# Kernel optimization log

Measured on AMD Instinct MI355X. Metric: run time of the kernel, lower is better.

The kernel has to match this reference:

```python
import jax, jax.numpy as jnp
import numpy as np

B, H, W, C = 4, 64, 64, 1280
NH = 16          # num heads
HD = C // NH     # 80 features per head
WS = 14          # window size
REL = 2 * WS - 1 # 27 relative-position entries per axis
EPS = 1e-6


def setup_inputs() -> dict:
    key = jax.random.key(0)
    ks = jax.random.split(key, 16)
    s = 0.02
    return {
        "imagelike_bhwc": jax.random.normal(ks[0], (B, H, W, C), jnp.float32),
        "ln1_g": jnp.ones((C,), jnp.float32),
        "ln1_b": jnp.zeros((C,), jnp.float32),
        "qkv_w": jax.random.normal(ks[1], (C, 3 * C), jnp.float32) * s,
        "qkv_b": jnp.zeros((3 * C,), jnp.float32),
        "proj_w": jax.random.normal(ks[2], (C, C), jnp.float32) * s,
        "proj_b": jnp.zeros((C,), jnp.float32),
        "rel_pos_h": jax.random.normal(ks[3], (REL, HD), jnp.float32) * s,
        "rel_pos_w": jax.random.normal(ks[4], (REL, HD), jnp.float32) * s,
        "ln2_g": jnp.ones((C,), jnp.float32),
        "ln2_b": jnp.zeros((C,), jnp.float32),
        "mlp_w1": jax.random.normal(ks[5], (C, 4 * C), jnp.float32) * s,
        "mlp_b1": jnp.zeros((4 * C,), jnp.float32),
        "mlp_w2": jax.random.normal(ks[6], (4 * C, C), jnp.float32) * s,
        "mlp_b2": jnp.zeros((C,), jnp.float32),
    }


def _layernorm(t, g, b):
    mu = jnp.mean(t, axis=-1, keepdims=True)
    var = jnp.var(t, axis=-1, keepdims=True)
    return (t - mu) * jax.lax.rsqrt(var + EPS) * g + b


def reference(imagelike_bhwc, ln1_g, ln1_b, qkv_w, qkv_b, proj_w, proj_b,
              rel_pos_h, rel_pos_w, ln2_g, ln2_b, mlp_w1, mlp_b1, mlp_w2, mlp_b2):
    x = imagelike_bhwc
    b, h, w, c = x.shape
    hd = c // NH
    scale = hd ** -0.5
    # --- image -> windows (pad to multiple of WS) ---
    hp, wp = (-h) % WS, (-w) % WS
    xp = jnp.pad(x, ((0, 0), (0, hp), (0, wp), (0, 0)))
    Hp, Wp = h + hp, w + wp
    ny, nx = Hp // WS, Wp // WS
    win = xp.reshape(b, ny, WS, nx, WS, c).transpose(0, 1, 3, 2, 4, 5)
    win = win.reshape(b * ny * nx, WS, WS, c)      # (Bw, S, S, C)
    Bw, N = win.shape[0], WS * WS
    # --- pre-attention layernorm + qkv ---
    t = _layernorm(win, ln1_g, ln1_b)
    qkv = t.reshape(Bw, N, c) @ qkv_w + qkv_b      # (Bw, N, 3C)
    qkv = qkv.reshape(Bw, N, 3, NH, hd).transpose(2, 0, 3, 1, 4)  # (3,Bw,NH,N,hd)
    q, k, v = qkv[0], qkv[1], qkv[2]
    # --- scores + decomposed relative position bias ---
    attn = jnp.einsum('bhqd,bhkd->bhqk', q * scale, k)            # (Bw,NH,N,N)
    idx = jnp.arange(WS)[:, None] - jnp.arange(WS)[None, :] + (WS - 1)
    Rh = rel_pos_h[idx]                                           # (WS,WS,hd)
    Rw = rel_pos_w[idx]                                           # (WS,WS,hd)
    qr = q.reshape(Bw, NH, WS, WS, hd)
    bias_h = jnp.einsum('bnyxd,ykd->bnyxk', qr, Rh)               # (Bw,NH,WS,WS,WS)
    bias_w = jnp.einsum('bnyxd,xkd->bnyxk', qr, Rw)
    bias = (bias_h[..., :, None] + bias_w[..., None, :]).reshape(Bw, NH, N, N)
    attn = jax.nn.softmax(attn + bias, axis=-1)
    out = jnp.einsum('bhqk,bhkd->bhqd', attn, v)                  # (Bw,NH,N,hd)
    out = out.transpose(0, 2, 1, 3).reshape(Bw, WS, WS, c)
    out = out @ proj_w + proj_b
    attn_out = out + win                                          # residual 1
    # --- MLP ---
    t2 = _layernorm(attn_out, ln2_g, ln2_b)
    mlp = jax.nn.gelu(t2 @ mlp_w1 + mlp_b1, approximate=False) @ mlp_w2 + mlp_b2
    out = mlp + attn_out                                          # residual 2
    # --- windows -> image (remove padding) ---
    img = out.reshape(b, ny, nx, WS, WS, c).transpose(0, 1, 3, 2, 4, 5)
    img = img.reshape(b, Hp, Wp, c)
    return img[:, :h, :w, :]
```

## Files before the change

### kernel.cpp

```cpp
#include <hip/hip_runtime.h>

typedef __attribute__((ext_vector_type(8))) short short8;
typedef __attribute__((ext_vector_type(4))) float f32x4;

#define GLBP(p) ((const __attribute__((address_space(1))) void*)(p))
#define LDSP(p) ((__attribute__((address_space(3))) void*)(p))

__device__ __forceinline__ float bf2f(unsigned short u) {
  return __uint_as_float(((unsigned int)u) << 16);
}
__device__ __forceinline__ unsigned short f2bf(float f) {
  unsigned int u = __float_as_uint(f);
  u += 0x7fff + ((u >> 16) & 1);
  return (unsigned short)(u >> 16);
}

__device__ __forceinline__ void tok2pix(int gt, int& b, int& py, int& px) {
  int w = gt / 196, t = gt - w * 196;
  b = w / 25;
  int wr = w - b * 25;
  int wy = wr / 5, wx = wr - wy * 5;
  int ty = t / 14;
  py = wy * 14 + ty;
  px = wx * 14 + (t - ty * 14);
}

__global__ void k_transpose(const float* __restrict__ W, unsigned short* __restrict__ Wt,
                            int K, int N) {
  __shared__ float tile[32][33];
  int tx = threadIdx.x, ty = threadIdx.y;
  int n0 = blockIdx.x * 32, k0 = blockIdx.y * 32;
#pragma unroll
  for (int i = 0; i < 4; ++i)
    tile[ty + 8 * i][tx] = W[(size_t)(k0 + ty + 8 * i) * N + n0 + tx];
  __syncthreads();
#pragma unroll
  for (int i = 0; i < 4; ++i)
    Wt[(size_t)(n0 + ty + 8 * i) * K + k0 + tx] = f2bf(tile[tx][ty + 8 * i]);
}

__global__ __launch_bounds__(256) void k_ln1(const float* __restrict__ x,
                                             const float* __restrict__ g,
                                             const float* __restrict__ be,
                                             unsigned short* __restrict__ A1,
                                             int w0, int ctok) {
  int m = blockIdx.x * 4 + (threadIdx.x >> 6);
  int lane = threadIdx.x & 63;
  int b, py, px;
  tok2pix(w0 * 196 + m, b, py, px);
  bool valid = (m < ctok) && (py < 64) && (px < 64);
  const float* row = x + ((size_t)((b * 64 + py) * 64 + px)) * 1280;
  float v[20];
#pragma unroll
  for (int i = 0; i < 20; ++i) v[i] = valid ? row[lane + 64 * i] : 0.f;
  float s = 0.f, ss = 0.f;
#pragma unroll
  for (int i = 0; i < 20; ++i) { s += v[i]; ss += v[i] * v[i]; }
#pragma unroll
  for (int o = 32; o > 0; o >>= 1) { s += __shfl_down(s, o); ss += __shfl_down(ss, o); }
  s = __shfl(s, 0);
  ss = __shfl(ss, 0);
  float mu = s * (1.f / 1280.f);
  float var = ss * (1.f / 1280.f) - mu * mu;
  float rinv = rsqrtf(var + 1e-6f);
  unsigned short* o1 = A1 + (size_t)m * 1280;
#pragma unroll
  for (int i = 0; i < 20; ++i) {
    int c = lane + 64 * i;
    o1[c] = f2bf((v[i] - mu) * rinv * g[c] + be[c]);
  }
}

__global__ __launch_bounds__(256) void k_ln2(const float* __restrict__ AT,
                                             const float* __restrict__ g,
                                             const float* __restrict__ be,
                                             unsigned short* __restrict__ A2,
                                             int w0, int ctok) {
  int m = blockIdx.x * 4 + (threadIdx.x >> 6);
  int lane = threadIdx.x & 63;
  int b, py, px;
  tok2pix(w0 * 196 + m, b, py, px);
  bool valid = (m < ctok) && (py < 64) && (px < 64);
  const float* row = AT + ((size_t)((b * 64 + py) * 64 + px)) * 1280;
  float v[20];
#pragma unroll
  for (int i = 0; i < 20; ++i) v[i] = valid ? row[lane + 64 * i] : 0.f;
  float s = 0.f, ss = 0.f;
#pragma unroll
  for (int i = 0; i < 20; ++i) { s += v[i]; ss += v[i] * v[i]; }
#pragma unroll
  for (int o = 32; o > 0; o >>= 1) { s += __shfl_down(s, o); ss += __shfl_down(ss, o); }
  s = __shfl(s, 0);
  ss = __shfl(ss, 0);
  float mu = s * (1.f / 1280.f);
  float var = ss * (1.f / 1280.f) - mu * mu;
  float rinv = rsqrtf(var + 1e-6f);
  unsigned short* o1 = A2 + (size_t)m * 1280;
#pragma unroll
  for (int i = 0; i < 20; ++i) {
    int c = lane + 64 * i;
    o1[c] = f2bf((v[i] - mu) * rinv * g[c] + be[c]);
  }
}

template <int EPI>
__device__ __forceinline__ void gemm_body(const unsigned short* __restrict__ A,
                                          const unsigned short* __restrict__ Bt,
                                          int K, int N, int gx,
                                          const float* __restrict__ bias,
                                          void* __restrict__ outp, int ctok) {
  __shared__ __align__(16) char smem[73728];
  int tid = threadIdx.x;
  int w = tid >> 6, lane = tid & 63;
  int nwg = gridDim.x, bid = blockIdx.x;
  int q = nwg >> 3, r = nwg & 7;
  int xcd = bid & 7, loc = bid >> 3;
  int wg = (xcd < r ? xcd * (q + 1) : r * (q + 1) + (xcd - r) * q) + loc;
  int bx = wg % gx, by = wg / gx;
  int mBase = by * 256, nBase = bx * 128;
  int wr = w >> 2, wc = w & 3;
  int la = lane & 15, lg = lane >> 4;

  int srow = tid >> 2;
  int schunk = (tid & 3) ^ ((srow >> 1) & 3);
  const char* pa0 = (const char*)A + (size_t)(mBase + srow) * K * 2 + (schunk << 4);
  const char* pa1 = (const char*)A + (size_t)(mBase + 128 + srow) * K * 2 + (schunk << 4);
  const char* pb0 = (const char*)Bt + (size_t)(nBase + srow) * K * 2 + (schunk << 4);
  int ldst = tid * 16;

  auto STAGE = [&](int slot, size_t ko) {
    int b = slot * 24576;
    __builtin_amdgcn_global_load_lds(GLBP(pa0 + ko), LDSP(smem + b + ldst), 16, 0, 0);
    __builtin_amdgcn_global_load_lds(GLBP(pa1 + ko), LDSP(smem + b + 8192 + ldst), 16, 0, 0);
    __builtin_amdgcn_global_load_lds(GLBP(pb0 + ko), LDSP(smem + b + 16384 + ldst), 16, 0, 0);
  };

  int offA[8], offB[2];
#pragma unroll
  for (int m = 0; m < 8; ++m) {
    int rr = wr * 128 + m * 16 + la;
    offA[m] = rr * 64 + ((lg ^ ((rr >> 1) & 3)) << 4);
  }
#pragma unroll
  for (int n = 0; n < 2; ++n) {
    int rr = wc * 32 + n * 16 + la;
    offB[n] = 16384 + rr * 64 + ((lg ^ ((rr >> 1) & 3)) << 4);
  }

  const f32x4 z4 = {0.f, 0.f, 0.f, 0.f};
  f32x4 acc[8][2];
#pragma unroll
  for (int m = 0; m < 8; ++m)
#pragma unroll
    for (int n = 0; n < 2; ++n) acc[m][n] = z4;

  int NT = K >> 5;
  STAGE(0, 0);
  STAGE(1, 64);
  int rs = 0;
  for (int t = 0; t < NT; ++t) {
    if (t + 1 < NT)
      asm volatile("s_waitcnt vmcnt(3)" ::: "memory");
    else
      asm volatile("s_waitcnt vmcnt(0)" ::: "memory");
    __builtin_amdgcn_s_barrier();
    __builtin_amdgcn_sched_barrier(0);
    if (t + 2 < NT) {
      int ws = rs + 2;
      if (ws >= 3) ws -= 3;
      STAGE(ws, (size_t)(t + 2) * 64);
    }
    const char* buf = (const char*)smem + rs * 24576;
    short8 af[4], bfr[2];
#pragma unroll
    for (int n = 0; n < 2; ++n) bfr[n] = *(const short8*)(buf + offB[n]);
#pragma unroll
    for (int m = 0; m < 4; ++m) af[m] = *(const short8*)(buf + offA[m]);
    __builtin_amdgcn_s_setprio(1);
#pragma unroll
    for (int m = 0; m < 4; ++m)
#pragma unroll
      for (int n = 0; n < 2; ++n)
        acc[m][n] = __builtin_amdgcn_mfma_f32_16x16x32_bf16(af[m], bfr[n], acc[m][n], 0, 0, 0);
    __builtin_amdgcn_s_setprio(0);
    __builtin_amdgcn_sched_barrier(0);
#pragma unroll
    for (int m = 0; m < 4; ++m) af[m] = *(const short8*)(buf + offA[m + 4]);
    __builtin_amdgcn_s_setprio(1);
#pragma unroll
    for (int m = 0; m < 4; ++m)
#pragma unroll
      for (int n = 0; n < 2; ++n)
        acc[m + 4][n] = __builtin_amdgcn_mfma_f32_16x16x32_bf16(af[m], bfr[n], acc[m + 4][n], 0, 0, 0);
    __builtin_amdgcn_s_setprio(0);
    rs = (rs == 2) ? 0 : rs + 1;
  }

#pragma unroll
  for (int m = 0; m < 8; ++m) {
#pragma unroll
    for (int n = 0; n < 2; ++n) {
      int col = nBase + wc * 32 + n * 16 + la;
      float bcol = bias[col];
#pragma unroll
      for (int j = 0; j < 4; ++j) {
        int row = mBase + wr * 128 + m * 16 + lg * 4 + j;
        float v = acc[m][n][j] + bcol;
        if (EPI == 0) {
          if (row < ctok) {
            int wloc = row / 196, tt = row - wloc * 196;
            int which = col / 1280, cr = col - which * 1280;
            int nh = cr / 80, d = cr - nh * 80;
            ((unsigned short*)outp)[((((size_t)wloc * 16 + nh) * 3 + which) * 196 + tt) * 80 + d] =
                f2bf(v);
          }
        } else {
          float gg = 0.5f * v * (1.f + erff(v * 0.70710678118654752f));
          ((unsigned short*)outp)[(size_t)row * N + col] = f2bf(gg);
        }
      }
    }
  }
}

template <int EPI>
__device__ __forceinline__ void gemm128_body(const unsigned short* __restrict__ A,
                                             const unsigned short* __restrict__ Bt,
                                             int K, int N, int gx,
                                             const float* __restrict__ bias,
                                             float* __restrict__ outp,
                                             const float* __restrict__ xres,
                                             int w0, int ctok) {
  __shared__ __align__(16) char smem[49152];
  int tid = threadIdx.x;
  int w = tid >> 6, lane = tid & 63;
  int nwg = gridDim.x, bid = blockIdx.x;
  int q = nwg >> 3, r = nwg & 7;
  int xcd = bid & 7, loc = bid >> 3;
  int wg = (xcd < r ? xcd * (q + 1) : r * (q + 1) + (xcd - r) * q) + loc;
  int bx = wg % gx, by = wg / gx;
  int mBase = by * 128, nBase = bx * 128;
  int wr = w >> 1, wc = w & 1;
  int la = lane & 15, lg = lane >> 4;

  int srow = tid >> 2;
  int schunk = (tid & 3) ^ ((srow >> 1) & 3);
  const char* pa[2];
  const char* pb[2];
#pragma unroll
  for (int i = 0; i < 2; ++i) {
    pa[i] = (const char*)A + (size_t)(mBase + srow + i * 64) * K * 2 + (schunk << 4);
    pb[i] = (const char*)Bt + (size_t)(nBase + srow + i * 64) * K * 2 + (schunk << 4);
  }
  int ldst = tid * 16;

  auto STAGE = [&](int slot, size_t ko) {
    int b = slot * 16384;
#pragma unroll
    for (int i = 0; i < 2; ++i)
      __builtin_amdgcn_global_load_lds(GLBP(pa[i] + ko), LDSP(smem + b + i * 4096 + ldst), 16, 0, 0);
#pragma unroll
    for (int i = 0; i < 2; ++i)
      __builtin_amdgcn_global_load_lds(GLBP(pb[i] + ko), LDSP(smem + b + 8192 + i * 4096 + ldst), 16, 0, 0);
  };

  int offA[4], offB[4];
#pragma unroll
  for (int m = 0; m < 4; ++m) {
    int rr = wr * 64 + m * 16 + la;
    offA[m] = rr * 64 + ((lg ^ ((rr >> 1) & 3)) << 4);
  }
#pragma unroll
  for (int n = 0; n < 4; ++n) {
    int rr = wc * 64 + n * 16 + la;
    offB[n] = 8192 + rr * 64 + ((lg ^ ((rr >> 1) & 3)) << 4);
  }

  const f32x4 z4 = {0.f, 0.f, 0.f, 0.f};
  f32x4 acc[4][4];
#pragma unroll
  for (int m = 0; m < 4; ++m)
#pragma unroll
    for (int n = 0; n < 4; ++n) acc[m][n] = z4;

  int NT = K >> 5;
  STAGE(0, 0);
  STAGE(1, 64);
  int rs = 0;
  for (int t = 0; t < NT; ++t) {
    if (t + 1 < NT)
      asm volatile("s_waitcnt vmcnt(4)" ::: "memory");
    else
      asm volatile("s_waitcnt vmcnt(0)" ::: "memory");
    __builtin_amdgcn_s_barrier();
    __builtin_amdgcn_sched_barrier(0);
    if (t + 2 < NT) {
      int ws = rs + 2;
      if (ws >= 3) ws -= 3;
      STAGE(ws, (size_t)(t + 2) * 64);
    }
    const char* buf = (const char*)smem + rs * 16384;
    short8 af[4], bfr[4];
#pragma unroll
    for (int n = 0; n < 4; ++n) bfr[n] = *(const short8*)(buf + offB[n]);
#pragma unroll
    for (int m = 0; m < 4; ++m) af[m] = *(const short8*)(buf + offA[m]);
    __builtin_amdgcn_s_setprio(1);
#pragma unroll
    for (int m = 0; m < 4; ++m)
#pragma unroll
      for (int n = 0; n < 4; ++n)
        acc[m][n] = __builtin_amdgcn_mfma_f32_16x16x32_bf16(af[m], bfr[n], acc[m][n], 0, 0, 0);
    __builtin_amdgcn_s_setprio(0);
    rs = (rs == 2) ? 0 : rs + 1;
  }

#pragma unroll
  for (int m = 0; m < 4; ++m) {
#pragma unroll
    for (int n = 0; n < 4; ++n) {
      int col = nBase + wc * 64 + n * 16 + la;
      float bcol = bias[col];
#pragma unroll
      for (int j = 0; j < 4; ++j) {
        int row = mBase + wr * 64 + m * 16 + lg * 4 + j;
        if (row < ctok) {
          int b, py, px;
          tok2pix(w0 * 196 + row, b, py, px);
          if (py < 64 && px < 64) {
            size_t pix = ((size_t)((b * 64 + py) * 64 + px)) * 1280 + col;
            float v = acc[m][n][j] + bcol;
            if (EPI == 1)
              outp[pix] = v + xres[pix];
            else
              outp[pix] = v + outp[pix];
          }
        }
      }
    }
  }
}

__global__ __launch_bounds__(512, 4) void k_gqkv(const unsigned short* A, const unsigned short* Bt,
                                                 int K, int N, int gx, const float* bias, void* o,
                                                 int ct) {
  gemm_body<0>(A, Bt, K, N, gx, bias, o, ct);
}
__global__ __launch_bounds__(512, 4) void k_gmlp1(const unsigned short* A, const unsigned short* Bt,
                                                  int K, int N, int gx, const float* bias, void* o,
                                                  int ct) {
  gemm_body<2>(A, Bt, K, N, gx, bias, o, ct);
}
__global__ __launch_bounds__(256, 3) void k_gproj(const unsigned short* A, const unsigned short* Bt,
                                                  int K, int N, int gx, const float* bias, float* o,
                                                  const float* xr, int w0, int ct) {
  gemm128_body<1>(A, Bt, K, N, gx, bias, o, xr, w0, ct);
}
__global__ __launch_bounds__(256, 3) void k_gmlp2(const unsigned short* A, const unsigned short* Bt,
                                                  int K, int N, int gx, const float* bias, float* o,
                                                  const float* xr, int w0, int ct) {
  gemm128_body<3>(A, Bt, K, N, gx, bias, o, xr, w0, ct);
}

__global__ __launch_bounds__(512, 1) void k_attn(const unsigned short* __restrict__ qkv,
                                                 const float* __restrict__ rph,
                                                 const float* __restrict__ rpw,
                                                 unsigned short* __restrict__ AO) {
  __shared__ unsigned short Ks[208 * 104];
  __shared__ unsigned short Vt[80 * 232];
  __shared__ unsigned short Ps[8][16 * 232];
  __shared__ unsigned short Bls[196 * 28];
  int wh = blockIdx.x;
  int w = wh >> 4, nh = wh & 15;
  int tid = threadIdx.x, wid = tid >> 6, lane = tid & 63;
  int la = lane & 15, lg = lane >> 4;
  const unsigned short* qb = qkv + (size_t)wh * 47040;
  const unsigned short* kb = qb + 15680;
  const unsigned short* vb = qb + 31360;
  const short8 z8 = {0, 0, 0, 0, 0, 0, 0, 0};

  for (int c = tid; c < 208 * 13; c += 512) {
    int t = c / 13, seg = c - t * 13;
    short8 kv = z8;
    if (t < 196 && seg < 10) kv = *(const short8*)(kb + (size_t)t * 80 + seg * 8);
    *(short8*)(Ks + t * 104 + seg * 8) = kv;
  }
  for (int c = tid; c < 1960; c += 512) {
    int t = c / 10, d8 = (c - t * 10) * 8;
    short8 vv = *(const short8*)(vb + (size_t)t * 80 + d8);
#pragma unroll
    for (int e = 0; e < 8; ++e) Vt[(d8 + e) * 232 + t] = (unsigned short)vv[e];
  }
  for (int i = tid; i < 80 * 36; i += 512) Vt[(i / 36) * 232 + 196 + (i % 36)] = 0;
  for (int id = tid; id < 196 * 28; id += 512) {
    int t = id / 28, c = id - t * 28;
    int y = t / 14, xx = t - y * 14;
    const float* R = (c < 14) ? (rph + (size_t)(y - c + 13) * 80)
                              : (rpw + (size_t)(xx - (c - 14) + 13) * 80);
    const unsigned short* qq = qb + (size_t)t * 80;
    float acc = 0.f;
#pragma unroll
    for (int d8 = 0; d8 < 10; ++d8) {
      short8 qv = *(const short8*)(qq + d8 * 8);
      const float4* Rv = (const float4*)(R + d8 * 8);
      float4 ra = Rv[0], rb = Rv[1];
      acc += bf2f((unsigned short)qv[0]) * ra.x + bf2f((unsigned short)qv[1]) * ra.y +
             bf2f((unsigned short)qv[2]) * ra.z + bf2f((unsigned short)qv[3]) * ra.w +
             bf2f((unsigned short)qv[4]) * rb.x + bf2f((unsigned short)qv[5]) * rb.y +
             bf2f((unsigned short)qv[6]) * rb.z + bf2f((unsigned short)qv[7]) * rb.w;
    }
    Bls[id] = f2bf(acc);
  }
  __syncthreads();

  int kyv[13], kxv[13];
#pragma unroll
  for (int ci = 0; ci < 13; ++ci) {
    int key = ci * 16 + la;
    kyv[ci] = key / 14;
    kxv[ci] = key - kyv[ci] * 14;
  }

  const float scale = 0.111803398874989485f;
  const f32x4 z4 = {0.f, 0.f, 0.f, 0.f};
  unsigned short* P = Ps[wid];

  auto process = [&](int rb) {
    short8 qa[3];
    int tq = rb * 16 + la;
    if (tq >= 196) tq = 0;
#pragma unroll
    for (int kk = 0; kk < 3; ++kk) {
      int d = kk * 32 + lg * 8;
      qa[kk] = (kk < 2 || lg < 2) ? *(const short8*)(qb + (size_t)tq * 80 + d) : z8;
    }
    f32x4 s[13];
#pragma unroll
    for (int i = 0; i < 13; ++i) s[i] = z4;
#pragma unroll
    for (int kk = 0; kk < 3; ++kk) {
#pragma unroll
      for (int ni = 0; ni < 13; ++ni) {
        short8 bb = *(const short8*)(Ks + (ni * 16 + la) * 104 + kk * 32 + lg * 8);
        s[ni] = __builtin_amdgcn_mfma_f32_16x16x32_bf16(qa[kk], bb, s[ni], 0, 0, 0);
      }
    }
#pragma unroll
    for (int j = 0; j < 4; ++j) {
      int rloc = lg * 4 + j;
      int t = rb * 16 + rloc;
      bool tval = t < 196;
      const unsigned short* Bp = Bls + (tval ? t : 0) * 28;
      float v[13];
      float mx = -3e30f;
#pragma unroll
      for (int ci = 0; ci < 13; ++ci) {
        int key = ci * 16 + la;
        float val = s[ci][j] * scale;
        if (key < 196 && tval) val += bf2f(Bp[kyv[ci]]) + bf2f(Bp[14 + kxv[ci]]);
        if (key >= 196 || !tval) val = -3e30f;
        v[ci] = val;
        mx = fmaxf(mx, val);
      }
#pragma unroll
      for (int o = 1; o < 16; o <<= 1) mx = fmaxf(mx, __shfl_xor(mx, o));
      float sum = 0.f;
#pragma unroll
      for (int ci = 0; ci < 13; ++ci) {
        float e = __expf(v[ci] - mx);
        v[ci] = e;
        sum += e;
      }
#pragma unroll
      for (int o = 1; o < 16; o <<= 1) sum += __shfl_xor(sum, o);
      float inv = 1.f / sum;
#pragma unroll
      for (int ci = 0; ci < 13; ++ci) P[rloc * 232 + ci * 16 + la] = f2bf(v[ci] * inv);
      P[rloc * 232 + 208 + la] = 0;
    }
    f32x4 o5[5];
#pragma unroll
    for (int i = 0; i < 5; ++i) o5[i] = z4;
#pragma unroll
    for (int kc = 0; kc < 7; ++kc) {
      short8 aa = *(const short8*)(P + la * 232 + kc * 32 + lg * 8);
#pragma unroll
      for (int ni = 0; ni < 5; ++ni) {
        short8 bb = *(const short8*)(Vt + (ni * 16 + la) * 232 + kc * 32 + lg * 8);
        o5[ni] = __builtin_amdgcn_mfma_f32_16x16x32_bf16(aa, bb, o5[ni], 0, 0, 0);
      }
    }
#pragma unroll
    for (int ni = 0; ni < 5; ++ni)
#pragma unroll
      for (int j = 0; j < 4; ++j) {
        int t = rb * 16 + lg * 4 + j;
        if (t < 196)
          AO[((size_t)w * 196 + t) * 1280 + nh * 80 + ni * 16 + la] = f2bf(o5[ni][j]);
      }
  };

  process(wid);
  if (wid < 5) process(wid + 8);
}

extern "C" void kernel_launch(void* const* d_in, const int* in_sizes, int n_in,
                              void* d_out, int out_size, void* d_ws, size_t ws_size,
                              hipStream_t stream) {
  const float* x = (const float*)d_in[0];
  const float* ln1g = (const float*)d_in[1];
  const float* ln1b = (const float*)d_in[2];
  const float* qkvw = (const float*)d_in[3];
  const float* qkvb = (const float*)d_in[4];
  const float* projw = (const float*)d_in[5];
  const float* projb = (const float*)d_in[6];
  const float* rph = (const float*)d_in[7];
  const float* rpw = (const float*)d_in[8];
  const float* ln2g = (const float*)d_in[9];
  const float* ln2b = (const float*)d_in[10];
  const float* w1 = (const float*)d_in[11];
  const float* b1 = (const float*)d_in[12];
  const float* w2 = (const float*)d_in[13];
  const float* b2 = (const float*)d_in[14];
  float* out = (float*)d_out;

  const size_t woff = (3840ull * 1280 + 1280ull * 1280 + 5120ull * 1280 + 1280ull * 5120) * 2;
  const int NWopts[12] = {25, 20, 18, 16, 14, 12, 10, 8, 5, 4, 2, 1};
  int NW = 0, Mb = 0;
  for (int i = 0; i < 12; ++i) {
    int nw = NWopts[i];
    int mb = ((nw * 196 + 255) / 256) * 256;
    size_t tot = woff + (size_t)mb * 12800;
    if (tot <= ws_size) { NW = nw; Mb = mb; break; }
  }
  if (!NW) return;

  char* p = (char*)d_ws;
  unsigned short* qkvwT = (unsigned short*)p; p += 3840ull * 1280 * 2;
  unsigned short* projwT = (unsigned short*)p; p += 1280ull * 1280 * 2;
  unsigned short* w1T = (unsigned short*)p; p += 5120ull * 1280 * 2;
  unsigned short* w2T = (unsigned short*)p; p += 1280ull * 5120 * 2;
  unsigned short* A1 = (unsigned short*)p; p += (size_t)Mb * 2560;
  unsigned short* QKV = (unsigned short*)p; p += (size_t)Mb * 7680;
  unsigned short* AO = (unsigned short*)p;
  unsigned short* Hb = QKV;
  unsigned short* A2 = A1;

  k_transpose<<<dim3(120, 40), dim3(32, 8), 0, stream>>>(qkvw, qkvwT, 1280, 3840);
  k_transpose<<<dim3(40, 40), dim3(32, 8), 0, stream>>>(projw, projwT, 1280, 1280);
  k_transpose<<<dim3(160, 40), dim3(32, 8), 0, stream>>>(w1, w1T, 1280, 5120);
  k_transpose<<<dim3(40, 160), dim3(32, 8), 0, stream>>>(w2, w2T, 5120, 1280);

  int gy256 = Mb / 256, gy128 = Mb / 128;
  int nchunks = (100 + NW - 1) / NW;
  for (int c = 0; c < nchunks; ++c) {
    int w0 = c * NW;
    int cw = (100 - w0 < NW) ? (100 - w0) : NW;
    int ctok = cw * 196;
    k_ln1<<<Mb / 4, 256, 0, stream>>>(x, ln1g, ln1b, A1, w0, ctok);
    k_gqkv<<<30 * gy256, 512, 0, stream>>>(A1, qkvwT, 1280, 3840, 30, qkvb, (void*)QKV, ctok);
    k_attn<<<cw * 16, 512, 0, stream>>>(QKV, rph, rpw, AO);
    k_gproj<<<10 * gy128, 256, 0, stream>>>(AO, projwT, 1280, 1280, 10, projb, out, x, w0, ctok);
    k_ln2<<<Mb / 4, 256, 0, stream>>>(out, ln2g, ln2b, A2, w0, ctok);
    k_gmlp1<<<40 * gy256, 512, 0, stream>>>(A2, w1T, 1280, 5120, 40, b1, (void*)Hb, ctok);
    k_gmlp2<<<10 * gy128, 256, 0, stream>>>(Hb, w2T, 5120, 1280, 10, b2, out, nullptr, w0, ctok);
  }
}
```

Measured before the change: 1.873 ms.

## Unify GEMMs on 128x128 tiles and split-K proj/mlp2 with atomic residual accumulation

Drops the 256x128 GEMM body and routes the qkv and mlp1 GEMMs through the 128x128 kernel. The proj GEMM now uses split-K 2 and mlp2 uses split-K 4, adding partial sums into the output with float atomicAdd. LN1 pre-writes x into the output buffer as the residual base, so the proj epilogue no longer reads x. This raises the workgroup count for the narrow N=1280 GEMMs to improve occupancy, at the cost of atomic traffic, nondeterministic summation order and smaller tiles on the wide GEMMs.

```diff
diff --git a/kernel.cpp b/kernel.cpp
--- a/kernel.cpp
+++ b/kernel.cpp
@@ -43,13 +43,15 @@
                                              const float* __restrict__ g,
                                              const float* __restrict__ be,
                                              unsigned short* __restrict__ A1,
+                                             float* __restrict__ outinit,
                                              int w0, int ctok) {
   int m = blockIdx.x * 4 + (threadIdx.x >> 6);
   int lane = threadIdx.x & 63;
   int b, py, px;
   tok2pix(w0 * 196 + m, b, py, px);
   bool valid = (m < ctok) && (py < 64) && (px < 64);
-  const float* row = x + ((size_t)((b * 64 + py) * 64 + px)) * 1280;
+  size_t pixrow = ((size_t)((b * 64 + py) * 64 + px)) * 1280;
+  const float* row = x + pixrow;
   float v[20];
 #pragma unroll
   for (int i = 0; i < 20; ++i) v[i] = valid ? row[lane + 64 * i] : 0.f;
@@ -64,10 +66,12 @@
   float var = ss * (1.f / 1280.f) - mu * mu;
   float rinv = rsqrtf(var + 1e-6f);
   unsigned short* o1 = A1 + (size_t)m * 1280;
+  float* oi = outinit + pixrow;
 #pragma unroll
   for (int i = 0; i < 20; ++i) {
     int c = lane + 64 * i;
     o1[c] = f2bf((v[i] - mu) * rinv * g[c] + be[c]);
+    if (valid) oi[c] = v[i];
   }
 }
 
@@ -103,133 +107,12 @@
   }
 }
 
-template <int EPI>
-__device__ __forceinline__ void gemm_body(const unsigned short* __restrict__ A,
-                                          const unsigned short* __restrict__ Bt,
-                                          int K, int N, int gx,
-                                          const float* __restrict__ bias,
-                                          void* __restrict__ outp, int ctok) {
-  __shared__ __align__(16) char smem[73728];
-  int tid = threadIdx.x;
-  int w = tid >> 6, lane = tid & 63;
-  int nwg = gridDim.x, bid = blockIdx.x;
-  int q = nwg >> 3, r = nwg & 7;
-  int xcd = bid & 7, loc = bid >> 3;
-  int wg = (xcd < r ? xcd * (q + 1) : r * (q + 1) + (xcd - r) * q) + loc;
-  int bx = wg % gx, by = wg / gx;
-  int mBase = by * 256, nBase = bx * 128;
-  int wr = w >> 2, wc = w & 3;
-  int la = lane & 15, lg = lane >> 4;
-
-  int srow = tid >> 2;
-  int schunk = (tid & 3) ^ ((srow >> 1) & 3);
-  const char* pa0 = (const char*)A + (size_t)(mBase + srow) * K * 2 + (schunk << 4);
-  const char* pa1 = (const char*)A + (size_t)(mBase + 128 + srow) * K * 2 + (schunk << 4);
-  const char* pb0 = (const char*)Bt + (size_t)(nBase + srow) * K * 2 + (schunk << 4);
-  int ldst = tid * 16;
-
-  auto STAGE = [&](int slot, size_t ko) {
-    int b = slot * 24576;
-    __builtin_amdgcn_global_load_lds(GLBP(pa0 + ko), LDSP(smem + b + ldst), 16, 0, 0);
-    __builtin_amdgcn_global_load_lds(GLBP(pa1 + ko), LDSP(smem + b + 8192 + ldst), 16, 0, 0);
-    __builtin_amdgcn_global_load_lds(GLBP(pb0 + ko), LDSP(smem + b + 16384 + ldst), 16, 0, 0);
-  };
-
-  int offA[8], offB[2];
-#pragma unroll
-  for (int m = 0; m < 8; ++m) {
-    int rr = wr * 128 + m * 16 + la;
-    offA[m] = rr * 64 + ((lg ^ ((rr >> 1) & 3)) << 4);
-  }
-#pragma unroll
-  for (int n = 0; n < 2; ++n) {
-    int rr = wc * 32 + n * 16 + la;
-    offB[n] = 16384 + rr * 64 + ((lg ^ ((rr >> 1) & 3)) << 4);
-  }
-
-  const f32x4 z4 = {0.f, 0.f, 0.f, 0.f};
-  f32x4 acc[8][2];
-#pragma unroll
-  for (int m = 0; m < 8; ++m)
-#pragma unroll
-    for (int n = 0; n < 2; ++n) acc[m][n] = z4;
-
-  int NT = K >> 5;
-  STAGE(0, 0);
-  STAGE(1, 64);
-  int rs = 0;
-  for (int t = 0; t < NT; ++t) {
-    if (t + 1 < NT)
-      asm volatile("s_waitcnt vmcnt(3)" ::: "memory");
-    else
-      asm volatile("s_waitcnt vmcnt(0)" ::: "memory");
-    __builtin_amdgcn_s_barrier();
-    __builtin_amdgcn_sched_barrier(0);
-    if (t + 2 < NT) {
-      int ws = rs + 2;
-      if (ws >= 3) ws -= 3;
-      STAGE(ws, (size_t)(t + 2) * 64);
-    }
-    const char* buf = (const char*)smem + rs * 24576;
-    short8 af[4], bfr[2];
-#pragma unroll
-    for (int n = 0; n < 2; ++n) bfr[n] = *(const short8*)(buf + offB[n]);
-#pragma unroll
-    for (int m = 0; m < 4; ++m) af[m] = *(const short8*)(buf + offA[m]);
-    __builtin_amdgcn_s_setprio(1);
-#pragma unroll
-    for (int m = 0; m < 4; ++m)
-#pragma unroll
-      for (int n = 0; n < 2; ++n)
-        acc[m][n] = __builtin_amdgcn_mfma_f32_16x16x32_bf16(af[m], bfr[n], acc[m][n], 0, 0, 0);
-    __builtin_amdgcn_s_setprio(0);
-    __builtin_amdgcn_sched_barrier(0);
-#pragma unroll
-    for (int m = 0; m < 4; ++m) af[m] = *(const short8*)(buf + offA[m + 4]);
-    __builtin_amdgcn_s_setprio(1);
-#pragma unroll
-    for (int m = 0; m < 4; ++m)
-#pragma unroll
-      for (int n = 0; n < 2; ++n)
-        acc[m + 4][n] = __builtin_amdgcn_mfma_f32_16x16x32_bf16(af[m], bfr[n], acc[m + 4][n], 0, 0, 0);
-    __builtin_amdgcn_s_setprio(0);
-    rs = (rs == 2) ? 0 : rs + 1;
-  }
-
-#pragma unroll
-  for (int m = 0; m < 8; ++m) {
-#pragma unroll
-    for (int n = 0; n < 2; ++n) {
-      int col = nBase + wc * 32 + n * 16 + la;
-      float bcol = bias[col];
-#pragma unroll
-      for (int j = 0; j < 4; ++j) {
-        int row = mBase + wr * 128 + m * 16 + lg * 4 + j;
-        float v = acc[m][n][j] + bcol;
-        if (EPI == 0) {
-          if (row < ctok) {
-            int wloc = row / 196, tt = row - wloc * 196;
-            int which = col / 1280, cr = col - which * 1280;
-            int nh = cr / 80, d = cr - nh * 80;
-            ((unsigned short*)outp)[((((size_t)wloc * 16 + nh) * 3 + which) * 196 + tt) * 80 + d] =
-                f2bf(v);
-          }
-        } else {
-          float gg = 0.5f * v * (1.f + erff(v * 0.70710678118654752f));
-          ((unsigned short*)outp)[(size_t)row * N + col] = f2bf(gg);
-        }
-      }
-    }
-  }
-}
-
-template <int EPI>
+template <int EPI, int SPLITK>
 __device__ __forceinline__ void gemm128_body(const unsigned short* __restrict__ A,
                                              const unsigned short* __restrict__ Bt,
-                                             int K, int N, int gx,
+                                             int Ktot, int N, int gx,
                                              const float* __restrict__ bias,
-                                             float* __restrict__ outp,
-                                             const float* __restrict__ xres,
+                                             void* __restrict__ outp,
                                              int w0, int ctok) {
   __shared__ __align__(16) char smem[49152];
   int tid = threadIdx.x;
@@ -238,8 +121,12 @@
   int q = nwg >> 3, r = nwg & 7;
   int xcd = bid & 7, loc = bid >> 3;
   int wg = (xcd < r ? xcd * (q + 1) : r * (q + 1) + (xcd - r) * q) + loc;
-  int bx = wg % gx, by = wg / gx;
+  int ntiles = nwg / SPLITK;
+  int kslice = wg / ntiles, tile = wg - kslice * ntiles;
+  int bx = tile % gx, by = tile / gx;
   int mBase = by * 128, nBase = bx * 128;
+  int K = Ktot / SPLITK;
+  int k0elem = kslice * K;
   int wr = w >> 1, wc = w & 1;
   int la = lane & 15, lg = lane >> 4;
 
@@ -249,8 +136,8 @@
   const char* pb[2];
 #pragma unroll
   for (int i = 0; i < 2; ++i) {
-    pa[i] = (const char*)A + (size_t)(mBase + srow + i * 64) * K * 2 + (schunk << 4);
-    pb[i] = (const char*)Bt + (size_t)(nBase + srow + i * 64) * K * 2 + (schunk << 4);
+    pa[i] = (const char*)A + ((size_t)(mBase + srow + i * 64) * Ktot + k0elem) * 2 + (schunk << 4);
+    pb[i] = (const char*)Bt + ((size_t)(nBase + srow + i * 64) * Ktot + k0elem) * 2 + (schunk << 4);
   }
   int ldst = tid * 16;
 
@@ -320,20 +207,28 @@
 #pragma unroll
     for (int n = 0; n < 4; ++n) {
       int col = nBase + wc * 64 + n * 16 + la;
-      float bcol = bias[col];
+      float bcol = (SPLITK == 1 || kslice == 0) ? bias[col] : 0.f;
 #pragma unroll
       for (int j = 0; j < 4; ++j) {
         int row = mBase + wr * 64 + m * 16 + lg * 4 + j;
-        if (row < ctok) {
-          int b, py, px;
-          tok2pix(w0 * 196 + row, b, py, px);
-          if (py < 64 && px < 64) {
-            size_t pix = ((size_t)((b * 64 + py) * 64 + px)) * 1280 + col;
-            float v = acc[m][n][j] + bcol;
-            if (EPI == 1)
-              outp[pix] = v + xres[pix];
-            else
-              outp[pix] = v + outp[pix];
+        float v = acc[m][n][j] + bcol;
+        if (EPI == 0) {
+          if (row < ctok) {
+            int wloc = row / 196, tt = row - wloc * 196;
+            int which = col / 1280, cr = col - which * 1280;
+            int nh = cr / 80, d = cr - nh * 80;
+            ((unsigned short*)outp)[((((size_t)wloc * 16 + nh) * 3 + which) * 196 + tt) * 80 + d] =
+                f2bf(v);
+          }
+        } else if (EPI == 2) {
+          float gg = 0.5f * v * (1.f + erff(v * 0.70710678118654752f));
+          ((unsigned short*)outp)[(size_t)row * N + col] = f2bf(gg);
+        } else {
+          if (row < ctok) {
+            int b, py, px;
+            tok2pix(w0 * 196 + row, b, py, px);
+            if (py < 64 && px < 64)
+              atomicAdd((float*)outp + ((size_t)((b * 64 + py) * 64 + px)) * 1280 + col, v);
           }
         }
       }
@@ -341,25 +236,25 @@
   }
 }
 
-__global__ __launch_bounds__(512, 4) void k_gqkv(const unsigned short* A, const unsigned short* Bt,
+__global__ __launch_bounds__(256, 3) void k_gqkv(const unsigned short* A, const unsigned short* Bt,
                                                  int K, int N, int gx, const float* bias, void* o,
-                                                 int ct) {
-  gemm_body<0>(A, Bt, K, N, gx, bias, o, ct);
-}
-__global__ __launch_bounds__(512, 4) void k_gmlp1(const unsigned short* A, const unsigned short* Bt,
+                                                 int w0, int ct) {
+  gemm128_body<0, 1>(A, Bt, K, N, gx, bias, o, w0, ct);
+}
+__global__ __launch_bounds__(256, 3) void k_gproj(const unsigned short* A, const unsigned short* Bt,
                                                   int K, int N, int gx, const float* bias, void* o,
-                                                  int ct) {
-  gemm_body<2>(A, Bt, K, N, gx, bias, o, ct);
-}
-__global__ __launch_bounds__(256, 3) void k_gproj(const unsigned short* A, const unsigned short* Bt,
-                                                  int K, int N, int gx, const float* bias, float* o,
-                                                  const float* xr, int w0, int ct) {
-  gemm128_body<1>(A, Bt, K, N, gx, bias, o, xr, w0, ct);
+                                                  int w0, int ct) {
+  gemm128_body<1, 2>(A, Bt, K, N, gx, bias, o, w0, ct);
+}
+__global__ __launch_bounds__(256, 3) void k_gmlp1(const unsigned short* A, const unsigned short* Bt,
+                                                  int K, int N, int gx, const float* bias, void* o,
+                                                  int w0, int ct) {
+  gemm128_body<2, 1>(A, Bt, K, N, gx, bias, o, w0, ct);
 }
 __global__ __launch_bounds__(256, 3) void k_gmlp2(const unsigned short* A, const unsigned short* Bt,
-                                                  int K, int N, int gx, const float* bias, float* o,
-                                                  const float* xr, int w0, int ct) {
-  gemm128_body<3>(A, Bt, K, N, gx, bias, o, xr, w0, ct);
+                                                  int K, int N, int gx, const float* bias, void* o,
+                                                  int w0, int ct) {
+  gemm128_body<3, 4>(A, Bt, K, N, gx, bias, o, w0, ct);
 }
 
 __global__ __launch_bounds__(512, 1) void k_attn(const unsigned short* __restrict__ qkv,
@@ -551,18 +446,18 @@
   k_transpose<<<dim3(160, 40), dim3(32, 8), 0, stream>>>(w1, w1T, 1280, 5120);
   k_transpose<<<dim3(40, 160), dim3(32, 8), 0, stream>>>(w2, w2T, 5120, 1280);
 
-  int gy256 = Mb / 256, gy128 = Mb / 128;
+  int gy = Mb / 128;
   int nchunks = (100 + NW - 1) / NW;
   for (int c = 0; c < nchunks; ++c) {
     int w0 = c * NW;
     int cw = (100 - w0 < NW) ? (100 - w0) : NW;
     int ctok = cw * 196;
-    k_ln1<<<Mb / 4, 256, 0, stream>>>(x, ln1g, ln1b, A1, w0, ctok);
-    k_gqkv<<<30 * gy256, 512, 0, stream>>>(A1, qkvwT, 1280, 3840, 30, qkvb, (void*)QKV, ctok);
+    k_ln1<<<Mb / 4, 256, 0, stream>>>(x, ln1g, ln1b, A1, out, w0, ctok);
+    k_gqkv<<<30 * gy, 256, 0, stream>>>(A1, qkvwT, 1280, 3840, 30, qkvb, (void*)QKV, w0, ctok);
     k_attn<<<cw * 16, 512, 0, stream>>>(QKV, rph, rpw, AO);
-    k_gproj<<<10 * gy128, 256, 0, stream>>>(AO, projwT, 1280, 1280, 10, projb, out, x, w0, ctok);
+    k_gproj<<<2 * 10 * gy, 256, 0, stream>>>(AO, projwT, 1280, 1280, 10, projb, (void*)out, w0, ctok);
     k_ln2<<<Mb / 4, 256, 0, stream>>>(out, ln2g, ln2b, A2, w0, ctok);
-    k_gmlp1<<<40 * gy256, 512, 0, stream>>>(A2, w1T, 1280, 5120, 40, b1, (void*)Hb, ctok);
-    k_gmlp2<<<10 * gy128, 256, 0, stream>>>(Hb, w2T, 5120, 1280, 10, b2, out, nullptr, w0, ctok);
-  }
-}
+    k_gmlp1<<<40 * gy, 256, 0, stream>>>(A2, w1T, 1280, 5120, 40, b1, (void*)Hb, w0, ctok);
+    k_gmlp2<<<4 * 10 * gy, 256, 0, stream>>>(Hb, w2T, 5120, 1280, 10, b2, (void*)out, w0, ctok);
+  }
+}
```

Measured after the change: 2.191 ms. +17.0%, slower.
